# Kernel optimization log

Hardware: AMD Instinct MI355X
Metric: run time of the kernel (lower is better)

The kernel has to match this reference:

```python
import jax, jax.numpy as jnp
import numpy as np

B, N = 1, 768
C_A, C_S, C_Z = 768, 384, 128
H, C_HID, N_TRANS = 16, 48, 2
INF = 1e9
PNAMES = ['attn_s_ln_g', 'attn_ada_gate_w', 'attn_ada_gate_b', 'attn_ada_skip_w',
          'wq', 'bq', 'wk', 'wv', 'z_ln_g', 'z_ln_b', 'wb', 'wg', 'wo',
          'attn_out_gate_w', 'attn_out_gate_b',
          'tr_s_ln_g', 'tr_ada_gate_w', 'tr_ada_gate_b', 'tr_ada_skip_w',
          'tr_w1', 'tr_w2', 'tr_wo', 'tr_out_gate_w', 'tr_out_gate_b']


def _ln(x, eps=1e-5):
    mu = jnp.mean(x, axis=-1, keepdims=True)
    var = jnp.mean((x - mu) ** 2, axis=-1, keepdims=True)
    return (x - mu) * jax.lax.rsqrt(var + eps)


def _adaln(a, s, s_g, gate_w, gate_b, skip_w):
    # AF3 Algorithm 26 AdaLN: a <- LN(a, no affine); s <- LN(s, scale only)
    a_ln = _ln(a)
    s_ln = _ln(s) * s_g
    return jax.nn.sigmoid(s_ln @ gate_w + gate_b) * a_ln + s_ln @ skip_w


def setup_inputs() -> dict:
    key = jax.random.key(0)
    ks = iter(jax.random.split(key, 40))
    w = lambda *sh: jax.random.normal(next(ks), sh, jnp.float32) * 0.02
    return dict(
        a=jax.random.normal(next(ks), (B, N, C_A), jnp.float32),
        s=jax.random.normal(next(ks), (B, N, C_S), jnp.float32),
        z=jax.random.normal(next(ks), (B, N, N, C_Z), jnp.float32),
        mask=jnp.ones((B, N), jnp.int32),
        attn_s_ln_g=jnp.ones((C_S,), jnp.float32),
        attn_ada_gate_w=w(C_S, C_A),
        attn_ada_gate_b=jnp.zeros((C_A,), jnp.float32),
        attn_ada_skip_w=w(C_S, C_A),
        wq=w(C_A, H * C_HID), bq=jnp.zeros((H * C_HID,), jnp.float32),
        wk=w(C_A, H * C_HID), wv=w(C_A, H * C_HID),
        z_ln_g=jnp.ones((C_Z,), jnp.float32), z_ln_b=jnp.zeros((C_Z,), jnp.float32),
        wb=w(C_Z, H), wg=w(C_A, H * C_HID), wo=w(H * C_HID, C_A),
        attn_out_gate_w=w(C_S, C_A),
        attn_out_gate_b=jnp.full((C_A,), -2.0, jnp.float32),  # AdaLN-Zero bias init -2
        tr_s_ln_g=jnp.ones((C_S,), jnp.float32),
        tr_ada_gate_w=w(C_S, C_A),
        tr_ada_gate_b=jnp.zeros((C_A,), jnp.float32),
        tr_ada_skip_w=w(C_S, C_A),
        tr_w1=w(C_A, N_TRANS * C_A), tr_w2=w(C_A, N_TRANS * C_A),
        tr_wo=w(N_TRANS * C_A, C_A),
        tr_out_gate_w=w(C_S, C_A),
        tr_out_gate_b=jnp.full((C_A,), -2.0, jnp.float32),
    )


def _block(a, s, z, maskf, p):
    # --- AttentionPairBias (AF3 Alg 24), residual ---
    a_ln = _adaln(a, s, p['attn_s_ln_g'], p['attn_ada_gate_w'],
                  p['attn_ada_gate_b'], p['attn_ada_skip_w'])
    q = (a_ln @ p['wq'] + p['bq']).reshape(B, N, H, C_HID)
    k = (a_ln @ p['wk']).reshape(B, N, H, C_HID)
    v = (a_ln @ p['wv']).reshape(B, N, H, C_HID)
    pair_bias = (_ln(z) * p['z_ln_g'] + p['z_ln_b']) @ p['wb']  # [B,N,N,H]
    logits = jnp.einsum('bqhc,bkhc->bhqk', q, k) / np.float32(np.sqrt(C_HID))
    logits = logits + jnp.moveaxis(pair_bias, -1, 1)
    logits = logits + (maskf - 1.0)[:, None, None, :] * INF  # mask over keys
    attn = jax.nn.softmax(logits, axis=-1)
    o = jnp.einsum('bhqk,bkhc->bqhc', attn, v)
    g = jax.nn.sigmoid(a_ln @ p['wg']).reshape(B, N, H, C_HID)
    o = (o * g).reshape(B, N, H * C_HID) @ p['wo']
    o = jax.nn.sigmoid(s @ p['attn_out_gate_w'] + p['attn_out_gate_b']) * o
    a = a + o
    # --- ConditionedTransitionBlock (AF3 Alg 25, SwiGLU), residual ---
    t_ln = _adaln(a, s, p['tr_s_ln_g'], p['tr_ada_gate_w'],
                  p['tr_ada_gate_b'], p['tr_ada_skip_w'])
    hid = jax.nn.silu(t_ln @ p['tr_w1']) * (t_ln @ p['tr_w2'])
    t = jax.nn.sigmoid(s @ p['tr_out_gate_w'] + p['tr_out_gate_b']) * (hid @ p['tr_wo'])
    t = t * maskf[..., None]  # _mask_trans=True
    return a + t


def reference(a, s, z, mask, attn_s_ln_g, attn_ada_gate_w, attn_ada_gate_b,
              attn_ada_skip_w, wq, bq, wk, wv, z_ln_g, z_ln_b, wb, wg, wo,
              attn_out_gate_w, attn_out_gate_b, tr_s_ln_g, tr_ada_gate_w,
              tr_ada_gate_b, tr_ada_skip_w, tr_w1, tr_w2, tr_wo,
              tr_out_gate_w, tr_out_gate_b):
    p = dict(zip(PNAMES, (attn_s_ln_g, attn_ada_gate_w, attn_ada_gate_b,
                          attn_ada_skip_w, wq, bq, wk, wv, z_ln_g, z_ln_b, wb,
                          wg, wo, attn_out_gate_w, attn_out_gate_b, tr_s_ln_g,
                          tr_ada_gate_w, tr_ada_gate_b, tr_ada_skip_w, tr_w1,
                          tr_w2, tr_wo, tr_out_gate_w, tr_out_gate_b)))
    return _block(a, s, z, mask.astype(a.dtype), p)
```

## Files before the change

### kernel.cpp

```cpp
#include <hip/hip_runtime.h>
#include <hip/hip_bf16.h>
#include <stdint.h>


typedef __bf16 bf16x8 __attribute__((ext_vector_type(8)));
typedef float  f32x4  __attribute__((ext_vector_type(4)));

#define DEVI __device__ __forceinline__

DEVI uint16_t f2b(float f){ __hip_bfloat16 h = __float2bfloat16(f); return __builtin_bit_cast(uint16_t, h); }
DEVI float    b2f(uint16_t u){ return __bfloat162float(__builtin_bit_cast(__hip_bfloat16, u)); }
DEVI float    sigm(float x){ return 1.0f/(1.0f + __expf(-x)); }

DEVI f32x4 MFMA(uint4 a, uint4 b, f32x4 c){
  return __builtin_amdgcn_mfma_f32_16x16x32_bf16(
      __builtin_bit_cast(bf16x8, a), __builtin_bit_cast(bf16x8, b), c, 0, 0, 0);
}

DEVI void glds16(const void* g, void* l){
  __builtin_amdgcn_global_load_lds(
      (const __attribute__((address_space(1))) void*)g,
      (__attribute__((address_space(3))) void*)l, 16, 0, 0);
}

constexpr size_t SZ_BT_ADA   = (size_t)1536*384*2;
constexpr size_t OFF_BT_ADA_ATTN = 0;
constexpr size_t OFF_BT_ADA_TR   = OFF_BT_ADA_ATTN + SZ_BT_ADA;
constexpr size_t OFF_BT_OUTGATE  = OFF_BT_ADA_TR   + SZ_BT_ADA;
constexpr size_t OFF_BT_QKVG     = OFF_BT_OUTGATE  + SZ_BT_ADA;
constexpr size_t OFF_BT_WO       = OFF_BT_QKVG + (size_t)3072*768*2;
constexpr size_t OFF_BT_W12      = OFF_BT_WO   + (size_t)768*768*2;
constexpr size_t OFF_BT_TRWO     = OFF_BT_W12  + (size_t)3072*768*2;
constexpr size_t OFF_WBGT        = OFF_BT_TRWO + (size_t)768*1536*2;
constexpr size_t OFF_ZCOL        = OFF_WBGT + 4096;
constexpr size_t OFF_OGB         = OFF_ZCOL + 256;
constexpr size_t OFF_SBF         = OFF_OGB + 6144;
constexpr size_t OFF_SLNA        = OFF_SBF  + (size_t)768*384*2;
constexpr size_t OFF_SLNT        = OFF_SLNA + (size_t)768*384*2;
constexpr size_t OFF_GATEOUT     = OFF_SLNT + (size_t)768*384*2;
constexpr size_t OFF_GSA         = OFF_GATEOUT + (size_t)768*1536*4;
constexpr size_t OFF_GST         = OFF_GSA + (size_t)768*1536*4;
constexpr size_t OFF_ALNBF       = OFF_GST + (size_t)768*1536*4;
constexpr size_t OFF_QP          = OFF_ALNBF + (size_t)768*768*2;
constexpr size_t OFF_KP          = OFF_QP + (size_t)16*768*48*2;
constexpr size_t OFF_VT          = OFF_KP + (size_t)16*768*48*2;
constexpr size_t OFF_GB          = OFF_VT + (size_t)16*48*768*2;
constexpr size_t OFF_BIASB       = OFF_GB + (size_t)768*768*2;
constexpr size_t OFF_OBF         = OFF_BIASB + (size_t)16*768*768*2;
constexpr size_t OFF_AMID        = OFF_OBF + (size_t)768*768*2;
constexpr size_t OFF_HID         = OFF_BIASB;

struct PreArgs {
  const float* src[14];
  uint16_t*    dst[14];
  int K[14], N[14], il[14];
  int prefix[15];
  int n_cvt;
  const float *s, *g_attn, *g_tr, *aogb, *togb, *zg, *zb, *wb;
  uint16_t *s_bf, *sln_a, *sln_t;
  float* ogb; uint16_t* wbgt; float* zcol;
};

__global__ __launch_bounds__(256) void k_pre(PreArgs a){
  __shared__ float lds[32][33];
  __shared__ float rs_[4], rq_[4];
  int bid = blockIdx.x, t = threadIdx.x;
  if (bid < a.n_cvt){
    int ti = 0;
    while (ti < 13 && bid >= a.prefix[ti+1]) ti++;
    int local = bid - a.prefix[ti];
    int K = a.K[ti], N = a.N[ti], il = a.il[ti];
    int tN = N >> 5;
    int n0 = (local % tN) << 5, k0 = (local / tN) << 5;
    const float* src = a.src[ti];
    uint16_t* dst = a.dst[ti];
    int c = t & 31, r0 = t >> 5;
    #pragma unroll
    for (int i = 0; i < 4; i++){
      int kk = r0 + 8*i;
      lds[kk][c] = src[(size_t)(k0+kk)*N + n0 + c];
    }
    __syncthreads();
    int rbase = (il == 0) ? n0 : (((n0 >> 5) << 6) + ((il == 2) ? 32 : 0));
    #pragma unroll
    for (int i = 0; i < 4; i++){
      int nn = r0 + 8*i;
      dst[(size_t)(rbase+nn)*K + k0 + c] = f2b(lds[c][nn]);
    }
    return;
  }
  int b = bid - a.n_cvt;
  if (b < 384){
    int row_id = b*2 + (t >> 7);
    int tt = t & 127;
    const float* row = a.s + (size_t)row_id*384;
    float x0 = row[tt], x1 = row[tt+128], x2 = row[tt+256];
    float sm = x0+x1+x2, sq = x0*x0+x1*x1+x2*x2;
    #pragma unroll
    for (int off = 32; off; off >>= 1){ sm += __shfl_xor(sm, off, 64); sq += __shfl_xor(sq, off, 64); }
    int w = t >> 6;
    if ((t & 63) == 0){ rs_[w] = sm; rq_[w] = sq; }
    __syncthreads();
    int base = (t >> 7)*2;
    float S = rs_[base]+rs_[base+1], Q = rq_[base]+rq_[base+1];
    float mu = S * (1.f/384.f);
    float var = Q * (1.f/384.f) - mu*mu;
    float rstd = rsqrtf(var + 1e-5f);
    float xs[3] = {x0, x1, x2};
    #pragma unroll
    for (int i = 0; i < 3; i++){
      int ci = tt + 128*i;
      float ln = (xs[i] - mu) * rstd;
      a.s_bf [(size_t)row_id*384 + ci] = f2b(xs[i]);
      a.sln_a[(size_t)row_id*384 + ci] = f2b(ln * a.g_attn[ci]);
      a.sln_t[(size_t)row_id*384 + ci] = f2b(ln * a.g_tr[ci]);
    }
  } else if (b == 384){
    for (int i = t; i < 1536; i += 256)
      a.ogb[i] = (i < 768) ? a.aogb[i] : a.togb[i-768];
  } else {
    for (int i = t; i < 2048; i += 256){
      int h = i >> 7, c = i & 127;
      a.wbgt[i] = f2b(a.zg[c] * a.wb[c*16 + h]);
    }
    if (t < 16){
      float cs = 0.f, cn = 0.f;
      for (int c = 0; c < 128; c++){ cs += a.zg[c]*a.wb[c*16+t]; cn += a.zb[c]*a.wb[c*16+t]; }
      a.zcol[t] = cs; a.zcol[16+t] = cn;
    }
  }
}

struct GemmP {
  const uint16_t *A, *BT;
  int N, K, gx, mode, gateLd, gateOff;
  float* outF; uint16_t* outB;
  const float *bias, *gate, *resid;
  const int* mask;
  uint16_t *qp, *kp, *vt, *gb;
  const float* bq;
};

DEVI void gemm_body(const GemmP& p, int bx, int by, uint16_t* As, uint16_t* Bs){
  int t = threadIdx.x;
  int n0 = bx*64, m0 = by*64;
  int w = t >> 6, lane = t & 63, mm = lane & 15, q = lane >> 4;
  int fc0 = 128*w + lane, fc1 = fc0 + 64;
  int r0 = fc0 >> 3, c0 = (fc0 & 7) ^ (r0 & 7);
  int r1 = fc1 >> 3, c1 = (fc1 & 7) ^ (r1 & 7);
  const uint16_t* gA0 = p.A  + (size_t)(m0 + r0)*p.K + c0*8;
  const uint16_t* gA1 = p.A  + (size_t)(m0 + r1)*p.K + c1*8;
  const uint16_t* gB0 = p.BT + (size_t)(n0 + r0)*p.K + c0*8;
  const uint16_t* gB1 = p.BT + (size_t)(n0 + r1)*p.K + c1*8;
  uint16_t* lA0 = As + (2*w + 0)*512;
  uint16_t* lA1 = As + (2*w + 1)*512;
  uint16_t* lB0 = Bs + (2*w + 0)*512;
  uint16_t* lB1 = Bs + (2*w + 1)*512;
  f32x4 zz = {0.f,0.f,0.f,0.f};
  f32x4 acc[4] = {zz, zz, zz, zz};
  int sw = mm & 7;
  for (int k0 = 0; k0 < p.K; k0 += 64){
    __syncthreads();
    glds16(gA0 + k0, lA0);
    glds16(gA1 + k0, lA1);
    glds16(gB0 + k0, lB0);
    glds16(gB1 + k0, lB1);
    __syncthreads();
    #pragma unroll
    for (int kc = 0; kc < 2; kc++){
      uint4 av = *(const uint4*)&As[(16*w + mm)*64 + ((kc*4 + q) ^ sw)*8];
      #pragma unroll
      for (int j = 0; j < 4; j++){
        uint4 bv = *(const uint4*)&Bs[(16*j + mm)*64 + ((kc*4 + q) ^ sw)*8];
        acc[j] = MFMA(av, bv, acc[j]);
      }
    }
  }
  if (p.mode == 6){
    #pragma unroll
    for (int jj = 0; jj < 2; jj++){
      #pragma unroll
      for (int rr = 0; rr < 4; rr++){
        int row = m0 + 16*w + q*4 + rr;
        int col = (n0 >> 1) + 16*jj + mm;
        float x1 = acc[jj][rr], x2 = acc[jj+2][rr];
        p.outB[(size_t)row*(p.N >> 1) + col] = f2b(x1*sigm(x1)*x2);
      }
    }
    return;
  }
  const float scale = 0.14433756729740643f;
  #pragma unroll
  for (int j = 0; j < 4; j++){
    #pragma unroll
    for (int rr = 0; rr < 4; rr++){
      int row = m0 + 16*w + q*4 + rr;
      int col = n0 + 16*j + mm;
      float v = acc[j][rr];
      size_t oi = (size_t)row*p.N + col;
      if (p.mode == 0)      p.outF[oi] = v;
      else if (p.mode == 2) p.outF[oi] = sigm(v + p.bias[col]);
      else if (p.mode == 5) p.outF[oi] = p.resid[oi] + p.gate[(size_t)row*p.gateLd + p.gateOff + col]*v;
      else if (p.mode == 4){
        float mf = (float)p.mask[row];
        p.outF[oi] = p.resid[oi] + mf * p.gate[(size_t)row*p.gateLd + p.gateOff + col] * v;
      } else {
        if (col < 768){
          int h = col/48, c = col - h*48;
          p.qp[((size_t)h*768 + row)*48 + c] = f2b((v + p.bq[col])*scale);
        } else if (col < 1536){
          int cc = col - 768; int h = cc/48, c = cc - h*48;
          p.kp[((size_t)h*768 + row)*48 + c] = f2b(v);
        } else if (col < 2304){
          int cc = col - 1536; int h = cc/48, c = cc - h*48;
          p.vt[((size_t)h*48 + c)*768 + row] = f2b(v);
        } else {
          p.gb[(size_t)row*768 + (col - 2304)] = f2b(v);
        }
      }
    }
  }
}

__global__ __launch_bounds__(256) void k_gemm(GemmP p){
  __shared__ __align__(16) uint16_t As[64*64], Bs[64*64];
  gemm_body(p, blockIdx.x, blockIdx.y, As, Bs);
}

DEVI void zbias_body(const float* __restrict__ z, const uint16_t* __restrict__ wbgt_g,
                     const float* __restrict__ zcol, uint16_t* __restrict__ bias_g,
                     int zbid, uint16_t* zb, uint16_t* wbt, float* mu_s, float* rs_s,
                     uint16_t* Sout)
{
  int t = threadIdx.x;
  int bx = zbid % 12, by = zbid / 12;
  size_t P0 = (size_t)by*768 + (size_t)bx*64;
  ((uint4*)wbt)[t] = ((const uint4*)wbgt_g)[t];
  int p = t >> 2, qq = t & 3;
  const float4* zp = (const float4*)(z + (P0 + p)*128) + qq*8;
  float s1 = 0.f, s2 = 0.f;
  uint32_t lb[16];
  #pragma unroll
  for (int it = 0; it < 8; it++){
    float4 v = zp[it];
    s1 += v.x + v.y + v.z + v.w;
    s2 += v.x*v.x + v.y*v.y + v.z*v.z + v.w*v.w;
    lb[2*it]   = (uint32_t)f2b(v.x) | ((uint32_t)f2b(v.y) << 16);
    lb[2*it+1] = (uint32_t)f2b(v.z) | ((uint32_t)f2b(v.w) << 16);
  }
  uint4* zb4 = (uint4*)zb;
  #pragma unroll
  for (int kk = 0; kk < 4; kk++)
    zb4[p*16 + qq*4 + kk] = ((uint4*)lb)[kk];
  s1 += __shfl_xor(s1, 1, 64); s1 += __shfl_xor(s1, 2, 64);
  s2 += __shfl_xor(s2, 1, 64); s2 += __shfl_xor(s2, 2, 64);
  if (qq == 0){
    float mu = s1 * (1.f/128.f);
    mu_s[p] = mu;
    rs_s[p] = rsqrtf(s2*(1.f/128.f) - mu*mu + 1e-5f);
  }
  __syncthreads();
  int w = t >> 6, lane = t & 63, hh = lane & 15, q = lane >> 4;
  float cs = zcol[hh], cn = zcol[16 + hh];
  f32x4 acc = {0.f, 0.f, 0.f, 0.f};
  const uint4* wbt4 = (const uint4*)wbt;
  #pragma unroll
  for (int kc = 0; kc < 4; kc++){
    uint4 av = zb4[(16*w + hh)*16 + kc*4 + q];
    uint4 bv = wbt4[hh*16 + kc*4 + q];
    acc = MFMA(av, bv, acc);
  }
  #pragma unroll
  for (int rr = 0; rr < 4; rr++){
    int pl = 16*w + q*4 + rr;
    float val = rs_s[pl]*(acc[rr] - mu_s[pl]*cs) + cn;
    Sout[hh*72 + pl] = f2b(val);
  }
  __syncthreads();
  int h2 = t >> 4, p2 = (t & 15)*4;
  uint2 v2 = *(uint2*)&Sout[h2*72 + p2];
  *(uint2*)(bias_g + (size_t)h2*589824 + P0 + p2) = v2;
}

struct ZbP { const float* z; const uint16_t* wbgt; const float* zcol; uint16_t* biasb; int off; };
struct FatArgs {
  GemmP g[3];
  int gstart[4];
  int gn, gtotal;
  ZbP zb;
};

union __align__(16) MegaLds {
  struct { uint16_t As[64*64], Bs[64*64]; } g;
  struct { uint16_t zb[64*128]; uint16_t wbt[16*128]; float mu[64], rs[64]; uint16_t Sout[16*72]; } z;
};

__global__ __launch_bounds__(256) void k_mega(FatArgs fa){
  __shared__ MegaLds L;
  int bid = blockIdx.x;
  if (bid >= fa.gtotal){
    zbias_body(fa.zb.z, fa.zb.wbgt, fa.zb.zcol, fa.zb.biasb, fa.zb.off + (bid - fa.gtotal),
               L.z.zb, L.z.wbt, L.z.mu, L.z.rs, L.z.Sout);
    return;
  }
  int gi = 0;
  while (gi + 1 < fa.gn && bid >= fa.gstart[gi+1]) gi++;
  GemmP p = fa.g[gi];
  int local = bid - fa.gstart[gi];
  gemm_body(p, local % p.gx, local / p.gx, L.g.As, L.g.Bs);
}

__global__ __launch_bounds__(256) void k_adaln2(
    const float* __restrict__ asrc, const float* __restrict__ gs,
    const float* __restrict__ gb, uint16_t* __restrict__ out)
{
  int b = blockIdx.x, t = threadIdx.x;
  const float* row = asrc + (size_t)b*768;
  float x0 = row[t], x1 = row[t+256], x2 = row[t+512];
  float sm = x0+x1+x2, sq = x0*x0+x1*x1+x2*x2;
  #pragma unroll
  for (int off = 32; off; off >>= 1){ sm += __shfl_xor(sm, off, 64); sq += __shfl_xor(sq, off, 64); }
  __shared__ float rs_[4], rq_[4];
  int w = t >> 6;
  if ((t & 63) == 0){ rs_[w] = sm; rq_[w] = sq; }
  __syncthreads();
  float S = rs_[0]+rs_[1]+rs_[2]+rs_[3], Q = rq_[0]+rq_[1]+rq_[2]+rq_[3];
  float mu = S*(1.f/768.f), var = Q*(1.f/768.f) - mu*mu, rstd = rsqrtf(var + 1e-5f);
  float xs[3] = {x0, x1, x2};
  #pragma unroll
  for (int i = 0; i < 3; i++){
    int c = t + 256*i;
    float g  = gs[(size_t)b*1536 + c];
    float sk = gs[(size_t)b*1536 + 768 + c];
    out[(size_t)b*768 + c] = f2b(sigm(g + gb[c]) * ((xs[i]-mu)*rstd) + sk);
  }
}

__global__ __launch_bounds__(256) void k_flash(
    const uint16_t* __restrict__ qp, const uint16_t* __restrict__ kp,
    const uint16_t* __restrict__ vt, const uint16_t* __restrict__ bias_g,
    const uint16_t* __restrict__ gb, const int* __restrict__ mask,
    uint16_t* __restrict__ obf)
{
  __shared__ __align__(16) uint16_t Qs[64*72], Ks[64*72], Vs[48*72], Ps[64*72], Bi[64*72];
  __shared__ float mk[768];
  int t = threadIdx.x;
  int q0 = blockIdx.x*64, h = blockIdx.y;
  int w = t >> 6, lane = t & 63, mm = lane & 15, q = lane >> 4;
  {
    const uint16_t* qbase = qp + ((size_t)h*768 + q0)*48;
    for (int i = t; i < 384; i += 256){
      int r = i/6, ch = i - r*6;
      *(uint4*)&Qs[r*72 + ch*8] = *(const uint4*)&qbase[r*48 + ch*8];
    }
    if (t < 128){
      uint4 z4; z4.x = z4.y = z4.z = z4.w = 0u;
      int r = t >> 1, off = 48 + (t & 1)*8;
      *(uint4*)&Qs[r*72 + off] = z4;
      *(uint4*)&Ks[r*72 + off] = z4;
    }
    mk[t] = (float)mask[t]; mk[t+256] = (float)mask[t+256]; mk[t+512] = (float)mask[t+512];
  }
  f32x4 zz = {0.f,0.f,0.f,0.f};
  f32x4 o0 = zz, o1 = zz, o2 = zz;
  f32x4 m_i = {-1e30f,-1e30f,-1e30f,-1e30f};
  f32x4 l_i = zz;
  const uint16_t* bbase0 = bias_g + (size_t)h*589824 + (size_t)q0*768;
  for (int kt = 0; kt < 12; kt++){
    __syncthreads();
    {
      const uint16_t* kbase = kp + ((size_t)h*768 + kt*64)*48;
      for (int i = t; i < 384; i += 256){
        int r = i/6, ch = i - r*6;
        *(uint4*)&Ks[r*72 + ch*8] = *(const uint4*)&kbase[r*48 + ch*8];
      }
      const uint16_t* vbase = vt + (size_t)h*48*768 + kt*64;
      for (int i = t; i < 384; i += 256){
        int r = i >> 3, ch = i & 7;
        *(uint4*)&Vs[r*72 + ch*8] = *(const uint4*)&vbase[(size_t)r*768 + ch*8];
      }
      const uint16_t* bbase = bbase0 + kt*64;
      for (int i = t; i < 512; i += 256){
        int r = i >> 3, ch = i & 7;
        *(uint4*)&Bi[r*72 + ch*8] = *(const uint4*)&bbase[(size_t)r*768 + ch*8];
      }
    }
    __syncthreads();
    f32x4 s[4] = {zz, zz, zz, zz};
    #pragma unroll
    for (int kc = 0; kc < 2; kc++){
      uint4 av = *(const uint4*)&Qs[(16*w + mm)*72 + kc*32 + q*8];
      #pragma unroll
      for (int j = 0; j < 4; j++){
        uint4 bv = *(const uint4*)&Ks[(16*j + mm)*72 + kc*32 + q*8];
        s[j] = MFMA(av, bv, s[j]);
      }
    }
    int rbase = 16*w + q*4;
    #pragma unroll
    for (int j = 0; j < 4; j++){
      int scol = kt*64 + 16*j + mm;
      float mt = (mk[scol] - 1.f)*1e9f;
      #pragma unroll
      for (int rr = 0; rr < 4; rr++)
        s[j][rr] += b2f(Bi[(rbase+rr)*72 + 16*j + mm]) + mt;
    }
    f32x4 tm = s[0];
    #pragma unroll
    for (int j = 1; j < 4; j++)
      #pragma unroll
      for (int rr = 0; rr < 4; rr++) tm[rr] = fmaxf(tm[rr], s[j][rr]);
    #pragma unroll
    for (int off = 1; off < 16; off <<= 1)
      #pragma unroll
      for (int rr = 0; rr < 4; rr++) tm[rr] = fmaxf(tm[rr], __shfl_xor(tm[rr], off, 64));
    f32x4 mnew, alpha, rsum = zz;
    #pragma unroll
    for (int rr = 0; rr < 4; rr++){
      mnew[rr] = fmaxf(m_i[rr], tm[rr]);
      alpha[rr] = __expf(m_i[rr] - mnew[rr]);
    }
    #pragma unroll
    for (int j = 0; j < 4; j++)
      #pragma unroll
      for (int rr = 0; rr < 4; rr++){
        s[j][rr] = __expf(s[j][rr] - mnew[rr]);
        rsum[rr] += s[j][rr];
      }
    #pragma unroll
    for (int off = 1; off < 16; off <<= 1)
      #pragma unroll
      for (int rr = 0; rr < 4; rr++) rsum[rr] += __shfl_xor(rsum[rr], off, 64);
    #pragma unroll
    for (int rr = 0; rr < 4; rr++){
      l_i[rr] = l_i[rr]*alpha[rr] + rsum[rr];
      o0[rr] *= alpha[rr]; o1[rr] *= alpha[rr]; o2[rr] *= alpha[rr];
      m_i[rr] = mnew[rr];
    }
    #pragma unroll
    for (int j = 0; j < 4; j++)
      #pragma unroll
      for (int rr = 0; rr < 4; rr++)
        Ps[(16*w + q*4 + rr)*72 + 16*j + mm] = f2b(s[j][rr]);
    __syncthreads();
    #pragma unroll
    for (int kc = 0; kc < 2; kc++){
      uint4 av = *(const uint4*)&Ps[(16*w + mm)*72 + kc*32 + q*8];
      uint4 bv0 = *(const uint4*)&Vs[(mm)*72      + kc*32 + q*8];
      uint4 bv1 = *(const uint4*)&Vs[(16+mm)*72   + kc*32 + q*8];
      uint4 bv2 = *(const uint4*)&Vs[(32+mm)*72   + kc*32 + q*8];
      o0 = MFMA(av, bv0, o0);
      o1 = MFMA(av, bv1, o1);
      o2 = MFMA(av, bv2, o2);
    }
  }
  f32x4 inv;
  #pragma unroll
  for (int rr = 0; rr < 4; rr++) inv[rr] = 1.f / l_i[rr];
  #pragma unroll
  for (int j = 0; j < 3; j++){
    f32x4 ov = (j == 0) ? o0 : (j == 1) ? o1 : o2;
    int col = 16*j + mm;
    #pragma unroll
    for (int rr = 0; rr < 4; rr++){
      int row = q0 + 16*w + q*4 + rr;
      float g = b2f(gb[(size_t)row*768 + h*48 + col]);
      obf[(size_t)row*768 + h*48 + col] = f2b(ov[rr]*inv[rr]*sigm(g));
    }
  }
}

extern "C" void kernel_launch(void* const* d_in, const int* in_sizes, int n_in,
                              void* d_out, int out_size, void* d_ws, size_t ws_size,
                              hipStream_t stream)
{
  const float* a            = (const float*)d_in[0];
  const float* s            = (const float*)d_in[1];
  const float* z            = (const float*)d_in[2];
  const int*   mask         = (const int*)  d_in[3];
  const float* attn_s_ln_g  = (const float*)d_in[4];
  const float* attn_gate_w  = (const float*)d_in[5];
  const float* attn_gate_b  = (const float*)d_in[6];
  const float* attn_skip_w  = (const float*)d_in[7];
  const float* wq           = (const float*)d_in[8];
  const float* bq           = (const float*)d_in[9];
  const float* wk           = (const float*)d_in[10];
  const float* wv           = (const float*)d_in[11];
  const float* z_ln_g       = (const float*)d_in[12];
  const float* z_ln_b       = (const float*)d_in[13];
  const float* wb           = (const float*)d_in[14];
  const float* wg           = (const float*)d_in[15];
  const float* wo           = (const float*)d_in[16];
  const float* attn_og_w    = (const float*)d_in[17];
  const float* attn_og_b    = (const float*)d_in[18];
  const float* tr_s_ln_g    = (const float*)d_in[19];
  const float* tr_gate_w    = (const float*)d_in[20];
  const float* tr_gate_b    = (const float*)d_in[21];
  const float* tr_skip_w    = (const float*)d_in[22];
  const float* tr_w1        = (const float*)d_in[23];
  const float* tr_w2        = (const float*)d_in[24];
  const float* tr_wo        = (const float*)d_in[25];
  const float* tr_og_w      = (const float*)d_in[26];
  const float* tr_og_b      = (const float*)d_in[27];

  char* wsb = (char*)d_ws;
  uint16_t* BTa   = (uint16_t*)(wsb + OFF_BT_ADA_ATTN);
  uint16_t* BTt   = (uint16_t*)(wsb + OFF_BT_ADA_TR);
  uint16_t* BTo   = (uint16_t*)(wsb + OFF_BT_OUTGATE);
  uint16_t* BTq   = (uint16_t*)(wsb + OFF_BT_QKVG);
  uint16_t* BTwo  = (uint16_t*)(wsb + OFF_BT_WO);
  uint16_t* BTw12 = (uint16_t*)(wsb + OFF_BT_W12);
  uint16_t* BTtw  = (uint16_t*)(wsb + OFF_BT_TRWO);
  uint16_t* WBGT  = (uint16_t*)(wsb + OFF_WBGT);
  float*    ZCOL  = (float*)   (wsb + OFF_ZCOL);
  float*    OGB   = (float*)   (wsb + OFF_OGB);
  uint16_t* SBF   = (uint16_t*)(wsb + OFF_SBF);
  uint16_t* SLNA  = (uint16_t*)(wsb + OFF_SLNA);
  uint16_t* SLNT  = (uint16_t*)(wsb + OFF_SLNT);
  float*    GATEOUT=(float*)   (wsb + OFF_GATEOUT);
  float*    GSA   = (float*)   (wsb + OFF_GSA);
  float*    GST   = (float*)   (wsb + OFF_GST);
  uint16_t* ALNBF = (uint16_t*)(wsb + OFF_ALNBF);
  uint16_t* QP    = (uint16_t*)(wsb + OFF_QP);
  uint16_t* KP    = (uint16_t*)(wsb + OFF_KP);
  uint16_t* VT    = (uint16_t*)(wsb + OFF_VT);
  uint16_t* GB    = (uint16_t*)(wsb + OFF_GB);
  uint16_t* BIASB = (uint16_t*)(wsb + OFF_BIASB);
  uint16_t* OBF   = (uint16_t*)(wsb + OFF_OBF);
  float*    AMID  = (float*)   (wsb + OFF_AMID);
  uint16_t* HIDBF = (uint16_t*)(wsb + OFF_HID);
  float*    OUTF  = (float*)d_out;

  PreArgs pa;
  const float* srcs[14] = {attn_gate_w, attn_skip_w, tr_gate_w, tr_skip_w,
                           attn_og_w, tr_og_w, wq, wk, wv, wg, wo, tr_w1, tr_w2, tr_wo};
  uint16_t* dsts[14] = {BTa, BTa + (size_t)768*384, BTt, BTt + (size_t)768*384,
                        BTo, BTo + (size_t)768*384,
                        BTq, BTq + (size_t)768*768, BTq + (size_t)2*768*768, BTq + (size_t)3*768*768,
                        BTwo, BTw12, BTw12, BTtw};
  int Ks[14] = {384,384,384,384,384,384, 768,768,768,768,768, 768,768, 1536};
  int Ns[14] = {768,768,768,768,768,768, 768,768,768,768,768, 1536,1536, 768};
  int il[14] = {0,0,0,0,0,0, 0,0,0,0,0, 1,2, 0};
  int tiles[14] = {288,288,288,288,288,288, 576,576,576,576,576, 1152,1152, 1152};
  int pre = 0;
  for (int i = 0; i < 14; i++){
    pa.src[i] = srcs[i]; pa.dst[i] = dsts[i]; pa.K[i] = Ks[i]; pa.N[i] = Ns[i]; pa.il[i] = il[i];
    pa.prefix[i] = pre; pre += tiles[i];
  }
  pa.prefix[14] = pre;
  pa.n_cvt = pre;
  pa.s = s; pa.g_attn = attn_s_ln_g; pa.g_tr = tr_s_ln_g;
  pa.aogb = attn_og_b; pa.togb = tr_og_b;
  pa.zg = z_ln_g; pa.zb = z_ln_b; pa.wb = wb;
  pa.s_bf = SBF; pa.sln_a = SLNA; pa.sln_t = SLNT;
  pa.ogb = OGB; pa.wbgt = WBGT; pa.zcol = ZCOL;
  k_pre<<<pre + 386, 256, 0, stream>>>(pa);

  FatArgs f2{};
  {
    GemmP p{};
    p.A = SBF; p.BT = BTo; p.N = 1536; p.K = 384; p.gx = 24; p.mode = 2;
    p.outF = GATEOUT; p.bias = OGB;
    f2.g[0] = p;
    p = GemmP{};
    p.A = SLNA; p.BT = BTa; p.N = 1536; p.K = 384; p.gx = 24; p.mode = 0; p.outF = GSA;
    f2.g[1] = p;
    p = GemmP{};
    p.A = SLNT; p.BT = BTt; p.N = 1536; p.K = 384; p.gx = 24; p.mode = 0; p.outF = GST;
    f2.g[2] = p;
    f2.gstart[0] = 0; f2.gstart[1] = 288; f2.gstart[2] = 576; f2.gstart[3] = 864;
    f2.gn = 3; f2.gtotal = 864;
    f2.zb = ZbP{z, WBGT, ZCOL, BIASB, 0};
  }
  k_mega<<<864 + 4608, 256, 0, stream>>>(f2);

  k_adaln2<<<768, 256, 0, stream>>>(a, GSA, attn_gate_b, ALNBF);

  FatArgs f4{};
  {
    GemmP p{};
    p.A = ALNBF; p.BT = BTq; p.N = 3072; p.K = 768; p.gx = 48; p.mode = 7;
    p.qp = QP; p.kp = KP; p.vt = VT; p.gb = GB; p.bq = bq;
    f4.g[0] = p;
    f4.gstart[0] = 0; f4.gstart[1] = 576; f4.gn = 1; f4.gtotal = 576;
    f4.zb = ZbP{z, WBGT, ZCOL, BIASB, 4608};
  }
  k_mega<<<576 + 4608, 256, 0, stream>>>(f4);

  k_flash<<<dim3(12,16), 256, 0, stream>>>(QP, KP, VT, BIASB, GB, mask, OBF);

  {
    GemmP p{};
    p.A = OBF; p.BT = BTwo; p.N = 768; p.K = 768; p.gx = 12; p.mode = 5;
    p.outF = AMID; p.gate = GATEOUT; p.gateLd = 1536; p.gateOff = 0; p.resid = a;
    k_gemm<<<dim3(12,12), 256, 0, stream>>>(p);
  }

  k_adaln2<<<768, 256, 0, stream>>>(AMID, GST, tr_gate_b, ALNBF);

  {
    GemmP p{};
    p.A = ALNBF; p.BT = BTw12; p.N = 3072; p.K = 768; p.gx = 48; p.mode = 6;
    p.outB = HIDBF;
    k_gemm<<<dim3(48,12), 256, 0, stream>>>(p);
  }

  {
    GemmP p{};
    p.A = HIDBF; p.BT = BTtw; p.N = 768; p.K = 1536; p.gx = 12; p.mode = 4;
    p.outF = OUTF; p.gate = GATEOUT; p.gateLd = 1536; p.gateOff = 768;
    p.resid = AMID; p.mask = mask;
    k_gemm<<<dim3(12,12), 256, 0, stream>>>(p);
  }
}
```

Measured before the change: 608.3 us.

## Use 128x128 GEMM tiles for wide projections and SwiGLU

```diff
diff --git a/kernel.cpp b/kernel.cpp
--- a/kernel.cpp
+++ b/kernel.cpp
@@ -176,20 +176,6 @@
       }
     }
   }
-  if (p.mode == 6){
-    #pragma unroll
-    for (int jj = 0; jj < 2; jj++){
-      #pragma unroll
-      for (int rr = 0; rr < 4; rr++){
-        int row = m0 + 16*w + q*4 + rr;
-        int col = (n0 >> 1) + 16*jj + mm;
-        float x1 = acc[jj][rr], x2 = acc[jj+2][rr];
-        p.outB[(size_t)row*(p.N >> 1) + col] = f2b(x1*sigm(x1)*x2);
-      }
-    }
-    return;
-  }
-  const float scale = 0.14433756729740643f;
   #pragma unroll
   for (int j = 0; j < 4; j++){
     #pragma unroll
@@ -199,24 +185,10 @@
       float v = acc[j][rr];
       size_t oi = (size_t)row*p.N + col;
       if (p.mode == 0)      p.outF[oi] = v;
-      else if (p.mode == 2) p.outF[oi] = sigm(v + p.bias[col]);
       else if (p.mode == 5) p.outF[oi] = p.resid[oi] + p.gate[(size_t)row*p.gateLd + p.gateOff + col]*v;
-      else if (p.mode == 4){
+      else {
         float mf = (float)p.mask[row];
         p.outF[oi] = p.resid[oi] + mf * p.gate[(size_t)row*p.gateLd + p.gateOff + col] * v;
-      } else {
-        if (col < 768){
-          int h = col/48, c = col - h*48;
-          p.qp[((size_t)h*768 + row)*48 + c] = f2b((v + p.bq[col])*scale);
-        } else if (col < 1536){
-          int cc = col - 768; int h = cc/48, c = cc - h*48;
-          p.kp[((size_t)h*768 + row)*48 + c] = f2b(v);
-        } else if (col < 2304){
-          int cc = col - 1536; int h = cc/48, c = cc - h*48;
-          p.vt[((size_t)h*48 + c)*768 + row] = f2b(v);
-        } else {
-          p.gb[(size_t)row*768 + (col - 2304)] = f2b(v);
-        }
       }
     }
   }
@@ -225,6 +197,107 @@
 __global__ __launch_bounds__(256) void k_gemm(GemmP p){
   __shared__ __align__(16) uint16_t As[64*64], Bs[64*64];
   gemm_body(p, blockIdx.x, blockIdx.y, As, Bs);
+}
+
+DEVI void gemm128_body(const GemmP& p, int bx, int by, uint16_t* As, uint16_t* Bs){
+  int t = threadIdx.x;
+  int n0 = bx*128, m0 = by*128;
+  int w = t >> 6, lane = t & 63, mm = lane & 15, q = lane >> 4;
+  int wm = w >> 1, wn = w & 1;
+  int sw = mm & 7;
+  const uint16_t* gA[4]; const uint16_t* gB[4];
+  uint16_t* lA[4]; uint16_t* lB[4];
+  #pragma unroll
+  for (int i = 0; i < 4; i++){
+    int fc = 256*w + 64*i + lane;
+    int r = fc >> 3, c = (fc & 7) ^ (r & 7);
+    gA[i] = p.A  + (size_t)(m0 + r)*p.K + c*8;
+    gB[i] = p.BT + (size_t)(n0 + r)*p.K + c*8;
+    lA[i] = As + (size_t)(256*w + 64*i)*8;
+    lB[i] = Bs + (size_t)(256*w + 64*i)*8;
+  }
+  f32x4 zz = {0.f,0.f,0.f,0.f};
+  f32x4 acc[4][4];
+  #pragma unroll
+  for (int m = 0; m < 4; m++)
+    #pragma unroll
+    for (int n = 0; n < 4; n++) acc[m][n] = zz;
+  for (int k0 = 0; k0 < p.K; k0 += 64){
+    __syncthreads();
+    #pragma unroll
+    for (int i = 0; i < 4; i++){
+      glds16(gA[i] + k0, lA[i]);
+      glds16(gB[i] + k0, lB[i]);
+    }
+    __syncthreads();
+    #pragma unroll
+    for (int kc = 0; kc < 2; kc++){
+      int co = ((kc*4 + q) ^ sw)*8;
+      uint4 av[4];
+      #pragma unroll
+      for (int m = 0; m < 4; m++)
+        av[m] = *(const uint4*)&As[(wm*64 + m*16 + mm)*64 + co];
+      #pragma unroll
+      for (int n = 0; n < 4; n++){
+        uint4 bv = *(const uint4*)&Bs[(wn*64 + n*16 + mm)*64 + co];
+        #pragma unroll
+        for (int m = 0; m < 4; m++)
+          acc[m][n] = MFMA(av[m], bv, acc[m][n]);
+      }
+    }
+  }
+  if (p.mode == 6){
+    int cbase = ((n0 >> 6) + wn)*32;
+    #pragma unroll
+    for (int m = 0; m < 4; m++){
+      #pragma unroll
+      for (int j = 0; j < 2; j++){
+        #pragma unroll
+        for (int rr = 0; rr < 4; rr++){
+          int row = m0 + wm*64 + m*16 + q*4 + rr;
+          int col = cbase + j*16 + mm;
+          float x1 = acc[m][j][rr], x2 = acc[m][j+2][rr];
+          p.outB[(size_t)row*1536 + col] = f2b(x1*sigm(x1)*x2);
+        }
+      }
+    }
+    return;
+  }
+  const float scale = 0.14433756729740643f;
+  #pragma unroll
+  for (int m = 0; m < 4; m++){
+    #pragma unroll
+    for (int n = 0; n < 4; n++){
+      #pragma unroll
+      for (int rr = 0; rr < 4; rr++){
+        int row = m0 + wm*64 + m*16 + q*4 + rr;
+        int col = n0 + wn*64 + n*16 + mm;
+        float v = acc[m][n][rr];
+        size_t oi = (size_t)row*p.N + col;
+        if (p.mode == 0)      p.outF[oi] = v;
+        else if (p.mode == 2) p.outF[oi] = sigm(v + p.bias[col]);
+        else {
+          if (col < 768){
+            int h = col/48, c = col - h*48;
+            p.qp[((size_t)h*768 + row)*48 + c] = f2b((v + p.bq[col])*scale);
+          } else if (col < 1536){
+            int cc = col - 768; int h = cc/48, c = cc - h*48;
+            p.kp[((size_t)h*768 + row)*48 + c] = f2b(v);
+          } else if (col < 2304){
+            int cc = col - 1536; int h = cc/48, c = cc - h*48;
+            p.vt[((size_t)h*48 + c)*768 + row] = f2b(v);
+          } else {
+            p.gb[(size_t)row*768 + (col - 2304)] = f2b(v);
+          }
+        }
+      }
+    }
+  }
+}
+
+__global__ __launch_bounds__(256) void k_gemm128(GemmP p){
+  __shared__ __align__(16) uint16_t As[128*64], Bs[128*64];
+  gemm128_body(p, blockIdx.x, blockIdx.y, As, Bs);
 }
 
 DEVI void zbias_body(const float* __restrict__ z, const uint16_t* __restrict__ wbgt_g,
@@ -291,7 +364,7 @@
 };
 
 union __align__(16) MegaLds {
-  struct { uint16_t As[64*64], Bs[64*64]; } g;
+  struct { uint16_t As[128*64], Bs[128*64]; } g;
   struct { uint16_t zb[64*128]; uint16_t wbt[16*128]; float mu[64], rs[64]; uint16_t Sout[16*72]; } z;
 };
 
@@ -307,7 +380,7 @@
   while (gi + 1 < fa.gn && bid >= fa.gstart[gi+1]) gi++;
   GemmP p = fa.g[gi];
   int local = bid - fa.gstart[gi];
-  gemm_body(p, local % p.gx, local / p.gx, L.g.As, L.g.Bs);
+  gemm128_body(p, local % p.gx, local / p.gx, L.g.As, L.g.Bs);
 }
 
 __global__ __launch_bounds__(256) void k_adaln2(
@@ -559,33 +632,33 @@
   FatArgs f2{};
   {
     GemmP p{};
-    p.A = SBF; p.BT = BTo; p.N = 1536; p.K = 384; p.gx = 24; p.mode = 2;
+    p.A = SBF; p.BT = BTo; p.N = 1536; p.K = 384; p.gx = 12; p.mode = 2;
     p.outF = GATEOUT; p.bias = OGB;
     f2.g[0] = p;
     p = GemmP{};
-    p.A = SLNA; p.BT = BTa; p.N = 1536; p.K = 384; p.gx = 24; p.mode = 0; p.outF = GSA;
+    p.A = SLNA; p.BT = BTa; p.N = 1536; p.K = 384; p.gx = 12; p.mode = 0; p.outF = GSA;
     f2.g[1] = p;
     p = GemmP{};
-    p.A = SLNT; p.BT = BTt; p.N = 1536; p.K = 384; p.gx = 24; p.mode = 0; p.outF = GST;
+    p.A = SLNT; p.BT = BTt; p.N = 1536; p.K = 384; p.gx = 12; p.mode = 0; p.outF = GST;
     f2.g[2] = p;
-    f2.gstart[0] = 0; f2.gstart[1] = 288; f2.gstart[2] = 576; f2.gstart[3] = 864;
-    f2.gn = 3; f2.gtotal = 864;
+    f2.gstart[0] = 0; f2.gstart[1] = 72; f2.gstart[2] = 144; f2.gstart[3] = 216;
+    f2.gn = 3; f2.gtotal = 216;
     f2.zb = ZbP{z, WBGT, ZCOL, BIASB, 0};
   }
-  k_mega<<<864 + 4608, 256, 0, stream>>>(f2);
+  k_mega<<<216 + 4608, 256, 0, stream>>>(f2);
 
   k_adaln2<<<768, 256, 0, stream>>>(a, GSA, attn_gate_b, ALNBF);
 
   FatArgs f4{};
   {
     GemmP p{};
-    p.A = ALNBF; p.BT = BTq; p.N = 3072; p.K = 768; p.gx = 48; p.mode = 7;
+    p.A = ALNBF; p.BT = BTq; p.N = 3072; p.K = 768; p.gx = 24; p.mode = 7;
     p.qp = QP; p.kp = KP; p.vt = VT; p.gb = GB; p.bq = bq;
     f4.g[0] = p;
-    f4.gstart[0] = 0; f4.gstart[1] = 576; f4.gn = 1; f4.gtotal = 576;
+    f4.gstart[0] = 0; f4.gstart[1] = 144; f4.gn = 1; f4.gtotal = 144;
     f4.zb = ZbP{z, WBGT, ZCOL, BIASB, 4608};
   }
-  k_mega<<<576 + 4608, 256, 0, stream>>>(f4);
+  k_mega<<<144 + 4608, 256, 0, stream>>>(f4);
 
   k_flash<<<dim3(12,16), 256, 0, stream>>>(QP, KP, VT, BIASB, GB, mask, OBF);
 
@@ -600,9 +673,9 @@
 
   {
     GemmP p{};
-    p.A = ALNBF; p.BT = BTw12; p.N = 3072; p.K = 768; p.gx = 48; p.mode = 6;
+    p.A = ALNBF; p.BT = BTw12; p.N = 3072; p.K = 768; p.gx = 24; p.mode = 6;
     p.outB = HIDBF;
-    k_gemm<<<dim3(48,12), 256, 0, stream>>>(p);
+    k_gemm128<<<dim3(24,6), 256, 0, stream>>>(p);
   }
 
   {
```

Result: no change. 614.7 us (+1.0%).

## Defer large weight conversions into mega kernel and coalesce V-transpose stores via LDS

Applied to the files above, without the earlier changes.

```diff
diff --git a/kernel.cpp b/kernel.cpp
--- a/kernel.cpp
+++ b/kernel.cpp
@@ -49,12 +49,36 @@
 constexpr size_t OFF_OBF         = OFF_BIASB + (size_t)16*768*768*2;
 constexpr size_t OFF_AMID        = OFF_OBF + (size_t)768*768*2;
 constexpr size_t OFF_HID         = OFF_BIASB;
+constexpr size_t WS_NEEDED       = OFF_AMID + (size_t)768*768*4;
+
+extern "C" size_t kernel_workspace_size(void){ return (size_t)64 << 20; }
+
+DEVI void cvt_body(const float* src, uint16_t* dst, int K, int N, int il, int local,
+                   float (*lds)[33])
+{
+  int t = threadIdx.x;
+  int tN = N >> 5;
+  int n0 = (local % tN) << 5, k0 = (local / tN) << 5;
+  int c = t & 31, r0 = t >> 5;
+  #pragma unroll
+  for (int i = 0; i < 4; i++){
+    int kk = r0 + 8*i;
+    lds[kk][c] = src[(size_t)(k0+kk)*N + n0 + c];
+  }
+  __syncthreads();
+  int rbase = (il == 0) ? n0 : (((n0 >> 5) << 6) + ((il == 2) ? 32 : 0));
+  #pragma unroll
+  for (int i = 0; i < 4; i++){
+    int nn = r0 + 8*i;
+    dst[(size_t)(rbase+nn)*K + k0 + c] = f2b(lds[c][nn]);
+  }
+}
 
 struct PreArgs {
-  const float* src[14];
-  uint16_t*    dst[14];
-  int K[14], N[14], il[14];
-  int prefix[15];
+  const float* src[6];
+  uint16_t*    dst[6];
+  int K[6], N[6];
+  int prefix[7];
   int n_cvt;
   const float *s, *g_attn, *g_tr, *aogb, *togb, *zg, *zb, *wb;
   uint16_t *s_bf, *sln_a, *sln_t;
@@ -67,26 +91,8 @@
   int bid = blockIdx.x, t = threadIdx.x;
   if (bid < a.n_cvt){
     int ti = 0;
-    while (ti < 13 && bid >= a.prefix[ti+1]) ti++;
-    int local = bid - a.prefix[ti];
-    int K = a.K[ti], N = a.N[ti], il = a.il[ti];
-    int tN = N >> 5;
-    int n0 = (local % tN) << 5, k0 = (local / tN) << 5;
-    const float* src = a.src[ti];
-    uint16_t* dst = a.dst[ti];
-    int c = t & 31, r0 = t >> 5;
-    #pragma unroll
-    for (int i = 0; i < 4; i++){
-      int kk = r0 + 8*i;
-      lds[kk][c] = src[(size_t)(k0+kk)*N + n0 + c];
-    }
-    __syncthreads();
-    int rbase = (il == 0) ? n0 : (((n0 >> 5) << 6) + ((il == 2) ? 32 : 0));
-    #pragma unroll
-    for (int i = 0; i < 4; i++){
-      int nn = r0 + 8*i;
-      dst[(size_t)(rbase+nn)*K + k0 + c] = f2b(lds[c][nn]);
-    }
+    while (ti < 5 && bid >= a.prefix[ti+1]) ti++;
+    cvt_body(a.src[ti], a.dst[ti], a.K[ti], a.N[ti], 0, bid - a.prefix[ti], lds);
     return;
   }
   int b = bid - a.n_cvt;
@@ -189,6 +195,21 @@
     }
     return;
   }
+  if (p.mode == 7 && n0 >= 1536 && n0 < 2304){
+    __syncthreads();
+    #pragma unroll
+    for (int j = 0; j < 4; j++)
+      #pragma unroll
+      for (int rr = 0; rr < 4; rr++)
+        As[(16*j + mm)*72 + (16*w + q*4 + rr)] = f2b(acc[j][rr]);
+    __syncthreads();
+    int cl = t >> 2, ch = (t & 3)*16;
+    int gc = n0 - 1536 + cl, h = gc/48, c = gc - 48*h;
+    uint16_t* dst = p.vt + ((size_t)h*48 + c)*768 + m0 + ch;
+    *(uint4*)dst       = *(const uint4*)&As[cl*72 + ch];
+    *(uint4*)(dst + 8) = *(const uint4*)&As[cl*72 + ch + 8];
+    return;
+  }
   const float scale = 0.14433756729740643f;
   #pragma unroll
   for (int j = 0; j < 4; j++){
@@ -211,9 +232,6 @@
         } else if (col < 1536){
           int cc = col - 768; int h = cc/48, c = cc - h*48;
           p.kp[((size_t)h*768 + row)*48 + c] = f2b(v);
-        } else if (col < 2304){
-          int cc = col - 1536; int h = cc/48, c = cc - h*48;
-          p.vt[((size_t)h*48 + c)*768 + row] = f2b(v);
         } else {
           p.gb[(size_t)row*768 + (col - 2304)] = f2b(v);
         }
@@ -223,8 +241,8 @@
 }
 
 __global__ __launch_bounds__(256) void k_gemm(GemmP p){
-  __shared__ __align__(16) uint16_t As[64*64], Bs[64*64];
-  gemm_body(p, blockIdx.x, blockIdx.y, As, Bs);
+  __shared__ __align__(16) uint16_t AsBs[2*64*64];
+  gemm_body(p, blockIdx.x, blockIdx.y, AsBs, AsBs + 64*64);
 }
 
 DEVI void zbias_body(const float* __restrict__ z, const uint16_t* __restrict__ wbgt_g,
@@ -283,31 +301,48 @@
 }
 
 struct ZbP { const float* z; const uint16_t* wbgt; const float* zcol; uint16_t* biasb; int off; };
+struct CvtP {
+  const float* src[8];
+  uint16_t* dst[8];
+  int K[8], N[8], il[8];
+  int prefix[9];
+  int n;
+};
 struct FatArgs {
   GemmP g[3];
   int gstart[4];
-  int gn, gtotal;
+  int gn, gtotal, ztotal;
   ZbP zb;
+  CvtP cv;
 };
 
 union __align__(16) MegaLds {
   struct { uint16_t As[64*64], Bs[64*64]; } g;
   struct { uint16_t zb[64*128]; uint16_t wbt[16*128]; float mu[64], rs[64]; uint16_t Sout[16*72]; } z;
+  float cv[32][33];
 };
 
 __global__ __launch_bounds__(256) void k_mega(FatArgs fa){
   __shared__ MegaLds L;
   int bid = blockIdx.x;
-  if (bid >= fa.gtotal){
+  if (bid < fa.gtotal){
+    int gi = 0;
+    while (gi + 1 < fa.gn && bid >= fa.gstart[gi+1]) gi++;
+    GemmP p = fa.g[gi];
+    int local = bid - fa.gstart[gi];
+    gemm_body(p, local % p.gx, local / p.gx, L.g.As, L.g.Bs);
+    return;
+  }
+  if (bid < fa.gtotal + fa.ztotal){
     zbias_body(fa.zb.z, fa.zb.wbgt, fa.zb.zcol, fa.zb.biasb, fa.zb.off + (bid - fa.gtotal),
                L.z.zb, L.z.wbt, L.z.mu, L.z.rs, L.z.Sout);
     return;
   }
-  int gi = 0;
-  while (gi + 1 < fa.gn && bid >= fa.gstart[gi+1]) gi++;
-  GemmP p = fa.g[gi];
-  int local = bid - fa.gstart[gi];
-  gemm_body(p, local % p.gx, local / p.gx, L.g.As, L.g.Bs);
+  int cid = bid - fa.gtotal - fa.ztotal;
+  int ti = 0;
+  while (ti + 1 < fa.cv.n && cid >= fa.cv.prefix[ti+1]) ti++;
+  cvt_body(fa.cv.src[ti], fa.cv.dst[ti], fa.cv.K[ti], fa.cv.N[ti], fa.cv.il[ti],
+           cid - fa.cv.prefix[ti], L.cv);
 }
 
 __global__ __launch_bounds__(256) void k_adaln2(
@@ -532,29 +567,24 @@
   float*    OUTF  = (float*)d_out;
 
   PreArgs pa;
-  const float* srcs[14] = {attn_gate_w, attn_skip_w, tr_gate_w, tr_skip_w,
-                           attn_og_w, tr_og_w, wq, wk, wv, wg, wo, tr_w1, tr_w2, tr_wo};
-  uint16_t* dsts[14] = {BTa, BTa + (size_t)768*384, BTt, BTt + (size_t)768*384,
-                        BTo, BTo + (size_t)768*384,
-                        BTq, BTq + (size_t)768*768, BTq + (size_t)2*768*768, BTq + (size_t)3*768*768,
-                        BTwo, BTw12, BTw12, BTtw};
-  int Ks[14] = {384,384,384,384,384,384, 768,768,768,768,768, 768,768, 1536};
-  int Ns[14] = {768,768,768,768,768,768, 768,768,768,768,768, 1536,1536, 768};
-  int il[14] = {0,0,0,0,0,0, 0,0,0,0,0, 1,2, 0};
-  int tiles[14] = {288,288,288,288,288,288, 576,576,576,576,576, 1152,1152, 1152};
-  int pre = 0;
-  for (int i = 0; i < 14; i++){
-    pa.src[i] = srcs[i]; pa.dst[i] = dsts[i]; pa.K[i] = Ks[i]; pa.N[i] = Ns[i]; pa.il[i] = il[i];
-    pa.prefix[i] = pre; pre += tiles[i];
-  }
-  pa.prefix[14] = pre;
-  pa.n_cvt = pre;
+  {
+    const float* srcs[6] = {attn_gate_w, attn_skip_w, tr_gate_w, tr_skip_w, attn_og_w, tr_og_w};
+    uint16_t* dsts[6] = {BTa, BTa + (size_t)768*384, BTt, BTt + (size_t)768*384,
+                         BTo, BTo + (size_t)768*384};
+    int pre = 0;
+    for (int i = 0; i < 6; i++){
+      pa.src[i] = srcs[i]; pa.dst[i] = dsts[i]; pa.K[i] = 384; pa.N[i] = 768;
+      pa.prefix[i] = pre; pre += 288;
+    }
+    pa.prefix[6] = pre;
+    pa.n_cvt = pre;
+  }
   pa.s = s; pa.g_attn = attn_s_ln_g; pa.g_tr = tr_s_ln_g;
   pa.aogb = attn_og_b; pa.togb = tr_og_b;
   pa.zg = z_ln_g; pa.zb = z_ln_b; pa.wb = wb;
   pa.s_bf = SBF; pa.sln_a = SLNA; pa.sln_t = SLNT;
   pa.ogb = OGB; pa.wbgt = WBGT; pa.zcol = ZCOL;
-  k_pre<<<pre + 386, 256, 0, stream>>>(pa);
+  k_pre<<<pa.n_cvt + 386, 256, 0, stream>>>(pa);
 
   FatArgs f2{};
   {
@@ -570,9 +600,25 @@
     f2.g[2] = p;
     f2.gstart[0] = 0; f2.gstart[1] = 288; f2.gstart[2] = 576; f2.gstart[3] = 864;
     f2.gn = 3; f2.gtotal = 864;
+    f2.ztotal = 4608;
     f2.zb = ZbP{z, WBGT, ZCOL, BIASB, 0};
-  }
-  k_mega<<<864 + 4608, 256, 0, stream>>>(f2);
+    const float* csrc[8] = {wq, wk, wv, wg, wo, tr_w1, tr_w2, tr_wo};
+    uint16_t* cdst[8] = {BTq, BTq + (size_t)768*768, BTq + (size_t)2*768*768, BTq + (size_t)3*768*768,
+                         BTwo, BTw12, BTw12, BTtw};
+    int cK[8] = {768,768,768,768,768, 768,768, 1536};
+    int cN[8] = {768,768,768,768,768, 1536,1536, 768};
+    int cil[8] = {0,0,0,0,0, 1,2, 0};
+    int ct[8]  = {576,576,576,576,576, 1152,1152, 1152};
+    int cpre = 0;
+    for (int i = 0; i < 8; i++){
+      f2.cv.src[i] = csrc[i]; f2.cv.dst[i] = cdst[i];
+      f2.cv.K[i] = cK[i]; f2.cv.N[i] = cN[i]; f2.cv.il[i] = cil[i];
+      f2.cv.prefix[i] = cpre; cpre += ct[i];
+    }
+    f2.cv.prefix[8] = cpre;
+    f2.cv.n = 8;
+    k_mega<<<864 + 4608 + cpre, 256, 0, stream>>>(f2);
+  }
 
   k_adaln2<<<768, 256, 0, stream>>>(a, GSA, attn_gate_b, ALNBF);
 
@@ -583,9 +629,11 @@
     p.qp = QP; p.kp = KP; p.vt = VT; p.gb = GB; p.bq = bq;
     f4.g[0] = p;
     f4.gstart[0] = 0; f4.gstart[1] = 576; f4.gn = 1; f4.gtotal = 576;
+    f4.ztotal = 4608;
     f4.zb = ZbP{z, WBGT, ZCOL, BIASB, 4608};
-  }
-  k_mega<<<576 + 4608, 256, 0, stream>>>(f4);
+    f4.cv.n = 0;
+    k_mega<<<576 + 4608, 256, 0, stream>>>(f4);
+  }
 
   k_flash<<<dim3(12,16), 256, 0, stream>>>(QP, KP, VT, BIASB, GB, mask, OBF);
 
```

Result: no change. 602.5 us (-1.0%).
